# Kernel optimization log

Measured on AMD Instinct MI355X. Metric: run time of the kernel, lower is better.

The kernel has to match this reference:

```python
import jax, jax.numpy as jnp
import numpy as np

N, E = 50000, 800000
IN, HID, HEADS, OUT = 128, 32, 8, 40
D1 = HID * HEADS  # 256


def setup_inputs() -> dict:
    key = jax.random.key(0)
    ks = jax.random.split(key, 24)

    def w(k, fin, fout):
        return (jax.random.normal(k, (fin, fout), jnp.float32) / np.sqrt(fin)).astype(jnp.float32)

    def b(k, fout):
        return (jax.random.normal(k, (fout,), jnp.float32) * 0.02).astype(jnp.float32)

    inp = {
        "x": jax.random.normal(ks[0], (N, IN), jnp.float32),
        "edge_index": jax.random.randint(ks[1], (2, E), 0, N, dtype=jnp.int64),
        # layer 1: TransformerConv(IN -> HID, heads=HEADS, concat=True, beta=True)
        "q1w": w(ks[2], IN, D1), "q1b": b(ks[3], D1),
        "k1w": w(ks[4], IN, D1), "k1b": b(ks[5], D1),
        "v1w": w(ks[6], IN, D1), "v1b": b(ks[7], D1),
        "s1w": w(ks[8], IN, D1), "s1b": b(ks[9], D1),
        "b1w": w(ks[10], 3 * D1, 1),
        # layer 2: TransformerConv(D1 -> OUT, heads=1, concat=False, beta=True)
        "q2w": w(ks[11], D1, OUT), "q2b": b(ks[12], OUT),
        "k2w": w(ks[13], D1, OUT), "k2b": b(ks[14], OUT),
        "v2w": w(ks[15], D1, OUT), "v2b": b(ks[16], OUT),
        "s2w": w(ks[17], D1, OUT), "s2b": b(ks[18], OUT),
        "b2w": w(ks[19], 3 * OUT, 1),
    }
    return inp


def _tconv(x, src, dst, qw, qb, kw, kb, vw, vb, sw, sb, bw, heads, ch, concat):
    """PyG TransformerConv (no edge_attr, root_weight=True, beta=True), eval mode."""
    n = x.shape[0]
    q = (x @ qw + qb).reshape(n, heads, ch)
    k = (x @ kw + kb).reshape(n, heads, ch)
    v = (x @ vw + vb).reshape(n, heads, ch)
    # per-edge attention logits: message flows src(j) -> dst(i)
    alpha = jnp.einsum("ehc,ehc->eh", q[dst], k[src]) / np.sqrt(ch)  # [E,H]
    # segment softmax over incoming edges of each dst node
    amax = jax.ops.segment_max(alpha, dst, num_segments=n)  # [N,H]
    a = jnp.exp(alpha - amax[dst])
    asum = jax.ops.segment_sum(a, dst, num_segments=n)  # [N,H]
    attn = a / asum[dst]  # [E,H]
    # scatter-aggregate weighted values
    out = jax.ops.segment_sum(v[src] * attn[:, :, None], dst, num_segments=n)  # [N,H,C]
    out = out.reshape(n, heads * ch) if concat else out.mean(axis=1)
    skip = x @ sw + sb
    beta = jax.nn.sigmoid(jnp.concatenate([out, skip, out - skip], axis=-1) @ bw)  # [N,1]
    return beta * skip + (1.0 - beta) * out


def reference(x, edge_index, q1w, q1b, k1w, k1b, v1w, v1b, s1w, s1b, b1w,
              q2w, q2b, k2w, k2b, v2w, v2b, s2w, s2b, b2w):
    src, dst = edge_index[0], edge_index[1]
    h = jax.nn.elu(_tconv(x, src, dst, q1w, q1b, k1w, k1b, v1w, v1b, s1w, s1b, b1w, HEADS, HID, True))
    return _tconv(h, src, dst, q2w, q2b, k2w, k2b, v2w, v2b, s2w, s2b, b2w, 1, OUT, False)
```

## Files before the change

kernel.cpp:

```cpp
#include <hip/hip_runtime.h>
#include <cstdint>
#include <cstddef>

#define N_NODES 50000
#define N_EDGES 800000
#define IN_F    128
#define HID     32
#define HEADS   8
#define OUT_F   40
#define D1      256
#define W1COLS  1024
#define W2COLS  160
#define CAP     64

#define GFILL_B   3125
#define G1_BX     391
#define G1_BY     8
#define G1_GEMM_B (G1_BX * G1_BY)
#define G1_TOTAL  (GFILL_B + G1_GEMM_B)

typedef unsigned short ushortT;
typedef unsigned char  ucharT;
typedef unsigned long long ullT;
typedef unsigned short ushortx8 __attribute__((ext_vector_type(8)));
typedef __bf16 bf16x8 __attribute__((ext_vector_type(8)));
typedef float floatx4 __attribute__((ext_vector_type(4)));
typedef float floatx2 __attribute__((ext_vector_type(2)));

__device__ inline ushortT f2bf(float f) {
    union { float f; unsigned int u; } c; c.f = f;
    unsigned int r = c.u + 0x7FFFu + ((c.u >> 16) & 1u);
    return (ushortT)(r >> 16);
}
__device__ inline float bf2f(ushortT h) {
    union { unsigned int u; float f; } c; c.u = ((unsigned int)h) << 16; return c.f;
}

__device__ inline void g2lds16(const void* gptr, void* lptr) {
    __builtin_amdgcn_global_load_lds(
        (const __attribute__((address_space(1))) unsigned int*)gptr,
        (__attribute__((address_space(3))) unsigned int*)lptr,
        16, 0, 0);
}

#define PREP_CONV_B  6250
#define PREP_W1_B    512
#define PREP_W2_B    160
#define PREP_TOTAL_B (PREP_CONV_B + PREP_W1_B + PREP_W2_B)

__global__ __launch_bounds__(256) void k_prep(
        const float* __restrict__ x, ushortT* __restrict__ xb,
        const float* __restrict__ q1w, const float* __restrict__ k1w,
        const float* __restrict__ v1w, const float* __restrict__ s1w,
        const float* __restrict__ q1b, const float* __restrict__ k1b,
        const float* __restrict__ v1b, const float* __restrict__ s1b,
        ushortT* __restrict__ W1T, float* __restrict__ b1c,
        const float* __restrict__ q2w, const float* __restrict__ k2w,
        const float* __restrict__ v2w, const float* __restrict__ s2w,
        const float* __restrict__ q2b, const float* __restrict__ k2b,
        const float* __restrict__ v2b, const float* __restrict__ s2b,
        ushortT* __restrict__ W2T, float* __restrict__ b2c) {
    int b = blockIdx.x;
    int tid = threadIdx.x;
    if (b < PREP_CONV_B) {
        int i = b * 256 + tid;
        float4 v = reinterpret_cast<const float4*>(x)[i];
        ushort4 o;
        o.x = f2bf(v.x); o.y = f2bf(v.y); o.z = f2bf(v.z); o.w = f2bf(v.w);
        reinterpret_cast<ushort4*>(xb)[i] = o;
    } else if (b < PREP_CONV_B + PREP_W1_B) {
        int t = (b - PREP_CONV_B) * 256 + tid;
        int c = t / IN_F, k = t % IN_F;
        int sel = c >> 8, cc = c & 255;
        const float* w = sel == 0 ? q1w : sel == 1 ? k1w : sel == 2 ? v1w : s1w;
        W1T[(size_t)c * IN_F + k] = f2bf(w[(size_t)k * D1 + cc]);
        if (k == 0) {
            const float* bb = sel == 0 ? q1b : sel == 1 ? k1b : sel == 2 ? v1b : s1b;
            b1c[c] = bb[cc];
        }
    } else {
        int t = (b - PREP_CONV_B - PREP_W1_B) * 256 + tid;
        int c = t / D1, k = t % D1;
        int sel = c / OUT_F, cc = c % OUT_F;
        const float* w = sel == 0 ? q2w : sel == 1 ? k2w : sel == 2 ? v2w : s2w;
        W2T[(size_t)c * D1 + k] = f2bf(w[(size_t)k * OUT_F + cc]);
        if (k == 0) {
            const float* bb = sel == 0 ? q2b : sel == 1 ? k2b : sel == 2 ? v2b : s2b;
            b2c[c] = bb[cc];
        }
    }
}

template<int MODE>
__global__ __launch_bounds__(256) void gemm_mfma_pack(
        const ushortT* __restrict__ A, const ushortT* __restrict__ BT,
        const float* __restrict__ bias, float* __restrict__ QSf,
        ushortT* __restrict__ QSh, ucharT* __restrict__ KV8,
        ushortT* __restrict__ K2V2,
        const int* __restrict__ ei, int* __restrict__ cursor, int* __restrict__ col,
        int M, int K, int Nn) {
    constexpr int TM = 128, TN = 128, TK = 32;
    __shared__ float smemf[4 * 1088];
    ushortT* As = reinterpret_cast<ushortT*>(smemf);
    ushortT* Bs = As + TM * TK;
    int bx2, by2;
    if (MODE == 1) {
        int t = blockIdx.x;
        int idx;
        bool isFill;
        if (t < 2 * GFILL_B) { isFill = !(t & 1); idx = t >> 1; }
        else                 { isFill = false;    idx = t - GFILL_B; }
        if (isFill) {
            int e = idx * 256 + threadIdx.x;
            if (e < N_EDGES) {
                int dd = ei[N_EDGES + e];
                int p = atomicAdd(&cursor[dd], 1);
                col[dd * CAP + p] = ei[e];
            }
            return;
        }
        bx2 = idx / G1_BY;
        by2 = idx % G1_BY;
    } else {
        bx2 = blockIdx.x;
        by2 = blockIdx.y;
    }
    int tid = threadIdx.x;
    int lane = tid & 63, wave = tid >> 6;
    int bm = bx2 * TM, bn = by2 * TN;
    int wm = (wave & 1) * 64, wn = (wave >> 1) * 64;
    int mrow = lane & 15, g = lane >> 4;
    int wbase = tid & ~63;
    int rsA0 = min(bm + (tid >> 2), M - 1);
    int rsA1 = min(bm + ((256 + tid) >> 2), M - 1);
    int rsB0 = min(bn + (tid >> 2), Nn - 1);
    int rsB1 = min(bn + ((256 + tid) >> 2), Nn - 1);
    int cs = (tid & 3) * 8;
    floatx4 acc[4][4] = {};

    for (int k0 = 0; k0 < K; k0 += TK) {
        g2lds16(A + (size_t)rsA0 * K + k0 + cs, (char*)As + (size_t)wbase * 16);
        g2lds16(A + (size_t)rsA1 * K + k0 + cs, (char*)As + (size_t)(256 + wbase) * 16);
        g2lds16(BT + (size_t)rsB0 * K + k0 + cs, (char*)Bs + (size_t)wbase * 16);
        g2lds16(BT + (size_t)rsB1 * K + k0 + cs, (char*)Bs + (size_t)(256 + wbase) * 16);
        __syncthreads();
        {
            bf16x8 a[4], b[4];
#pragma unroll
            for (int i = 0; i < 4; ++i)
                a[i] = *reinterpret_cast<const bf16x8*>(As + (wm + i * 16 + mrow) * TK + g * 8);
#pragma unroll
            for (int j = 0; j < 4; ++j)
                b[j] = *reinterpret_cast<const bf16x8*>(Bs + (wn + j * 16 + mrow) * TK + g * 8);
#pragma unroll
            for (int i = 0; i < 4; ++i)
#pragma unroll
                for (int j = 0; j < 4; ++j)
                    acc[i][j] = __builtin_amdgcn_mfma_f32_16x16x32_bf16(a[i], b[j], acc[i][j], 0, 0, 0);
        }
        __syncthreads();
    }

    if (MODE == 1) {
        float* lds = smemf + wave * 1088;
        int sec = by2 >> 1;
        int ccbase = (by2 & 1) * 128 + wn;
        int cb4 = (lane & 15) * 4;
        int rlo = lane >> 4;
        float4 bv = *reinterpret_cast<const float4*>(bias + by2 * 128 + wn + cb4);
#pragma unroll
        for (int i = 0; i < 4; ++i) {
#pragma unroll
            for (int j = 0; j < 4; ++j)
#pragma unroll
                for (int r = 0; r < 4; ++r)
                    lds[(g * 4 + r) * 68 + j * 16 + mrow] = acc[i][j][r];
#pragma unroll
            for (int it = 0; it < 4; ++it) {
                int row = it * 4 + rlo;
                int gm = bm + wm + i * 16 + row;
                if (gm >= M) continue;
                float4 v = *reinterpret_cast<float4*>(lds + row * 68 + cb4);
                v.x += bv.x; v.y += bv.y; v.z += bv.z; v.w += bv.w;
                int cc = ccbase + cb4;
                if (sec == 0 || sec == 3) {
                    ushort4 h;
                    h.x = f2bf(v.x); h.y = f2bf(v.y); h.z = f2bf(v.z); h.w = f2bf(v.w);
                    ushortT* dst = QSh + (size_t)gm * 512 + (sec == 3 ? 256 : 0) + cc;
                    *reinterpret_cast<ushort4*>(dst) = h;
                } else {
                    unsigned int pk = 0;
                    pk = __builtin_amdgcn_cvt_pk_fp8_f32(v.x, v.y, pk, false);
                    pk = __builtin_amdgcn_cvt_pk_fp8_f32(v.z, v.w, pk, true);
                    ucharT* dst = KV8 + (size_t)gm * 512 + (sec == 2 ? 256 : 0) + cc;
                    *reinterpret_cast<unsigned int*>(dst) = pk;
                }
            }
        }
    } else {
#pragma unroll
        for (int i = 0; i < 4; ++i) {
#pragma unroll
            for (int j = 0; j < 4; ++j) {
                int gn = bn + wn + j * 16 + mrow;
                if (gn >= Nn) continue;
                float bvs = bias[gn];
#pragma unroll
                for (int r = 0; r < 4; ++r) {
                    int gm = bm + wm + i * 16 + g * 4 + r;
                    if (gm >= M) continue;
                    float val = acc[i][j][r] + bvs;
                    int sec = gn / OUT_F, cc = gn % OUT_F;
                    if (sec == 0)      QSf[(size_t)gm * 80 + cc] = val;
                    else if (sec == 1) K2V2[(size_t)gm * 80 + cc] = f2bf(val);
                    else if (sec == 2) K2V2[(size_t)gm * 80 + 40 + cc] = f2bf(val);
                    else               QSf[(size_t)gm * 80 + 40 + cc] = val;
                }
            }
        }
    }
}

__global__ __launch_bounds__(256) void k_edge1(
        const ushortT* __restrict__ QSh, const ucharT* __restrict__ KV8,
        const float* __restrict__ bw,
        const int* __restrict__ degc, const int* __restrict__ col,
        ushortT* __restrict__ H1b) {
    int gid  = blockIdx.x * blockDim.x + threadIdx.x;
    int lane = threadIdx.x & 63;
    int node = __builtin_amdgcn_readfirstlane(gid >> 6);
    if (node >= N_NODES) return;
    const float scale = 0.17677669529663687f;
    bool isV = lane >= 32;
    ushortx8 qs8 = *reinterpret_cast<const ushortx8*>(QSh + (size_t)node * 512 + lane * 8);
    float qsc = isV ? 1.0f : scale;
    floatx2 q01, q23, q45, q67;
    q01[0] = bf2f(qs8[0]) * qsc; q01[1] = bf2f(qs8[1]) * qsc;
    q23[0] = bf2f(qs8[2]) * qsc; q23[1] = bf2f(qs8[3]) * qsc;
    q45[0] = bf2f(qs8[4]) * qsc; q45[1] = bf2f(qs8[5]) * qsc;
    q67[0] = bf2f(qs8[6]) * qsc; q67[1] = bf2f(qs8[7]) * qsc;

    float l = 0.f;
    floatx2 acc0 = {0.f, 0.f}, acc1 = {0.f, 0.f}, acc2 = {0.f, 0.f}, acc3 = {0.f, 0.f};
    const int* colp = col + node * CAP;
    int d = degc[node];
    int voff = lane * 8;

#define EDGE_BODY(kv) do {                                                              \
    floatx2 a0 = __builtin_amdgcn_cvt_pk_f32_fp8((unsigned)(kv), false);                \
    floatx2 a1 = __builtin_amdgcn_cvt_pk_f32_fp8((unsigned)(kv), true);                 \
    floatx2 a2 = __builtin_amdgcn_cvt_pk_f32_fp8((unsigned)((kv) >> 32), false);        \
    floatx2 a3 = __builtin_amdgcn_cvt_pk_f32_fp8((unsigned)((kv) >> 32), true);         \
    floatx2 pd = q01 * a0 + q23 * a1 + q45 * a2 + q67 * a3;                             \
    float p = pd[0] + pd[1];                                                            \
    p += __int_as_float(__builtin_amdgcn_update_dpp(                                    \
             0, __float_as_int(p), 0xB1, 0xF, 0xF, false));    \
    p += __int_as_float(__builtin_amdgcn_update_dpp(                                    \
             0, __float_as_int(p), 0x4E, 0xF, 0xF, false));    \
    float e = __expf(p);                                                                \
    float eb = __shfl(e, lane & 31);             \
    l += eb;                                                                            \
    floatx2 ev = {eb, eb};                                                              \
    acc0 += ev * a0; acc1 += ev * a1; acc2 += ev * a2; acc3 += ev * a3;                 \
} while (0)

    int t = 0;
    for (; t + 4 <= d; t += 4) {
        int4 js = *reinterpret_cast<const int4*>(colp + t);
        ullT kv0 = *reinterpret_cast<const ullT*>(KV8 + ((size_t)js.x << 9) + voff);
        ullT kv1 = *reinterpret_cast<const ullT*>(KV8 + ((size_t)js.y << 9) + voff);
        ullT kv2 = *reinterpret_cast<const ullT*>(KV8 + ((size_t)js.z << 9) + voff);
        ullT kv3 = *reinterpret_cast<const ullT*>(KV8 + ((size_t)js.w << 9) + voff);
        EDGE_BODY(kv0);
        EDGE_BODY(kv1);
        EDGE_BODY(kv2);
        EDGE_BODY(kv3);
    }
    for (; t < d; ++t) {
        int j = colp[t];
        ullT kv = *reinterpret_cast<const ullT*>(KV8 + ((size_t)j << 9) + voff);
        EDGE_BODY(kv);
    }
#undef EDGE_BODY

    float inv = (l > 0.f) ? 1.f / l : 0.f;
    floatx2 iv = {inv, inv};
    floatx2 o0 = acc0 * iv, o1 = acc1 * iv, o2 = acc2 * iv, o3 = acc3 * iv;
    int cb = isV ? (lane - 32) * 8 : 0;
    float4 wa0 = *reinterpret_cast<const float4*>(bw + cb);
    float4 wa1 = *reinterpret_cast<const float4*>(bw + cb + 4);
    float4 wb0 = *reinterpret_cast<const float4*>(bw + D1 + cb);
    float4 wb1 = *reinterpret_cast<const float4*>(bw + D1 + cb + 4);
    float4 wc0 = *reinterpret_cast<const float4*>(bw + 2 * D1 + cb);
    float4 wc1 = *reinterpret_cast<const float4*>(bw + 2 * D1 + cb + 4);
    float part = 0.f;
    if (isV) {
        part = o0[0] * wa0.x + o0[1] * wa0.y + o1[0] * wa0.z + o1[1] * wa0.w
             + o2[0] * wa1.x + o2[1] * wa1.y + o3[0] * wa1.z + o3[1] * wa1.w
             + q01[0] * wb0.x + q01[1] * wb0.y + q23[0] * wb0.z + q23[1] * wb0.w
             + q45[0] * wb1.x + q45[1] * wb1.y + q67[0] * wb1.z + q67[1] * wb1.w
             + (o0[0] - q01[0]) * wc0.x + (o0[1] - q01[1]) * wc0.y
             + (o1[0] - q23[0]) * wc0.z + (o1[1] - q23[1]) * wc0.w
             + (o2[0] - q45[0]) * wc1.x + (o2[1] - q45[1]) * wc1.y
             + (o3[0] - q67[0]) * wc1.z + (o3[1] - q67[1]) * wc1.w;
    }
#pragma unroll
    for (int s = 1; s < 32; s <<= 1) part += __shfl_xor(part, s);
    float beta = 1.f / (1.f + __expf(-part));
    if (isV) {
        float h[8];
        h[0] = beta * q01[0] + (1.f - beta) * o0[0];
        h[1] = beta * q01[1] + (1.f - beta) * o0[1];
        h[2] = beta * q23[0] + (1.f - beta) * o1[0];
        h[3] = beta * q23[1] + (1.f - beta) * o1[1];
        h[4] = beta * q45[0] + (1.f - beta) * o2[0];
        h[5] = beta * q45[1] + (1.f - beta) * o2[1];
        h[6] = beta * q67[0] + (1.f - beta) * o3[0];
        h[7] = beta * q67[1] + (1.f - beta) * o3[1];
        ushortx8 hb;
#pragma unroll
        for (int c = 0; c < 8; ++c) {
            float hv = h[c] > 0.f ? h[c] : __expf(h[c]) - 1.f;
            hb[c] = f2bf(hv);
        }
        *reinterpret_cast<ushortx8*>(H1b + (size_t)node * D1 + (lane - 32) * 8) = hb;
    }
}

__global__ __launch_bounds__(256) void k_edge2(
        const float* __restrict__ QS, const ushortT* __restrict__ K2V2,
        const float* __restrict__ bw,
        const int* __restrict__ degc, const int* __restrict__ col,
        float* __restrict__ out) {
    __shared__ float        qbuf[4][40];
    __shared__ float        attn[4][64];
    __shared__ int          jb[4][64];
    __shared__ unsigned int ksm[4][64 * 21];
    int gid  = blockIdx.x * blockDim.x + threadIdx.x;
    int node = gid >> 6;
    int wave = threadIdx.x >> 6;
    int lane = threadIdx.x & 63;
    if (node >= N_NODES) return;
    const float scale = 0.15811388300841897f;
    bool act = lane < OUT_F;
    if (act) qbuf[wave][lane] = QS[(size_t)node * 80 + lane] * scale;

    int d = degc[node];
    if (lane < d) jb[wave][lane] = col[node * CAP + lane];

    const unsigned int* Kdw = reinterpret_cast<const unsigned int*>(K2V2);
    int sr = lane / 20;
    int sc = lane - sr * 20;
    for (int r0 = 0; r0 < d; r0 += 3) {
        int rr = r0 + sr;
        if (lane < 60 && rr < d)
            ksm[wave][rr * 21 + sc] = Kdw[(size_t)jb[wave][rr] * 40 + sc];
    }

    float p = 0.f;
    if (lane < d) {
        float s = 0.f;
#pragma unroll
        for (int c = 0; c < 20; ++c) {
            unsigned int kk = ksm[wave][lane * 21 + c];
            s += qbuf[wave][2 * c]     * bf2f((ushortT)(kk & 0xFFFFu))
               + qbuf[wave][2 * c + 1] * bf2f((ushortT)(kk >> 16));
        }
        p = __expf(s);
    }
    attn[wave][lane] = p;
    float l = p;
#pragma unroll
    for (int s = 1; s < 64; s <<= 1) l += __shfl_xor(l, s);

    float acc = 0.f;
    int ln = act ? lane : 0;
    int e = 0;
    for (; e + 4 <= d; e += 4) {
        int je0 = jb[wave][e],     je1 = jb[wave][e + 1];
        int je2 = jb[wave][e + 2], je3 = jb[wave][e + 3];
        float v0 = bf2f(K2V2[(size_t)je0 * 80 + 40 + ln]);
        float v1 = bf2f(K2V2[(size_t)je1 * 80 + 40 + ln]);
        float v2 = bf2f(K2V2[(size_t)je2 * 80 + 40 + ln]);
        float v3 = bf2f(K2V2[(size_t)je3 * 80 + 40 + ln]);
        acc += (attn[wave][e] * v0 + attn[wave][e + 1] * v1)
             + (attn[wave][e + 2] * v2 + attn[wave][e + 3] * v3);
    }
    for (; e < d; ++e)
        acc += attn[wave][e] * bf2f(K2V2[(size_t)jb[wave][e] * 80 + 40 + ln]);

    float inv = (l > 0.f) ? 1.f / l : 0.f;
    float o  = acc * inv;
    float sk = act ? QS[(size_t)node * 80 + 40 + lane] : 0.f;
    float part = act ? (o * bw[lane] + sk * bw[OUT_F + lane] + (o - sk) * bw[2 * OUT_F + lane]) : 0.f;
#pragma unroll
    for (int s = 1; s < 64; s <<= 1) part += __shfl_xor(part, s);
    float beta = 1.f / (1.f + __expf(-part));
    if (act) out[(size_t)node * OUT_F + lane] = beta * sk + (1.f - beta) * o;
}

extern "C" void kernel_launch(void* const* d_in, const int* in_sizes, int n_in,
                              void* d_out, int out_size, void* d_ws, size_t ws_size,
                              hipStream_t stream) {
    const float* x   = (const float*)d_in[0];
    const int*   ei  = (const int*)d_in[1];
    const float* q1w = (const float*)d_in[2];
    const float* q1b = (const float*)d_in[3];
    const float* k1w = (const float*)d_in[4];
    const float* k1b = (const float*)d_in[5];
    const float* v1w = (const float*)d_in[6];
    const float* v1b = (const float*)d_in[7];
    const float* s1w = (const float*)d_in[8];
    const float* s1b = (const float*)d_in[9];
    const float* b1w = (const float*)d_in[10];
    const float* q2w = (const float*)d_in[11];
    const float* q2b = (const float*)d_in[12];
    const float* k2w = (const float*)d_in[13];
    const float* k2b = (const float*)d_in[14];
    const float* v2w = (const float*)d_in[15];
    const float* v2b = (const float*)d_in[16];
    const float* s2w = (const float*)d_in[17];
    const float* s2b = (const float*)d_in[18];
    const float* b2w = (const float*)d_in[19];
    float* out = (float*)d_out;

    char* w = (char*)d_ws;
    ushortT* QSh = (ushortT*)w;
    ucharT*  KV8 = (ucharT*)(w + 51200000);
    ushortT* H1b = (ushortT*)(w + 102400000);
    ushortT* xb  = (ushortT*)(w + 128000000);
    ushortT* W1T = (ushortT*)(w + 140800000);
    ushortT* W2T = (ushortT*)(w + 141062144);
    float*   b1c = (float*)(w + 141144064);
    float*   b2c = (float*)(w + 141148160);
    int* cursor  = (int*)(w + 141149184);
    int* col     = cursor + N_NODES;
    float*   QS2  = (float*)w;
    ushortT* K2V2 = (ushortT*)(w + 51200000);

    hipMemsetAsync(cursor, 0, N_NODES * sizeof(int), stream);

    k_prep<<<PREP_TOTAL_B, 256, 0, stream>>>(
        x, xb,
        q1w, k1w, v1w, s1w, q1b, k1b, v1b, s1b, W1T, b1c,
        q2w, k2w, v2w, s2w, q2b, k2b, v2b, s2b, W2T, b2c);

    gemm_mfma_pack<1><<<G1_TOTAL, 256, 0, stream>>>(
        xb, W1T, b1c, nullptr, QSh, KV8, nullptr,
        ei, cursor, col, N_NODES, IN_F, W1COLS);

    k_edge1<<<(N_NODES * 64) / 256, 256, 0, stream>>>(QSh, KV8, b1w, cursor, col, H1b);

    dim3 g2((N_NODES + 127) / 128, (W2COLS + 127) / 128);
    gemm_mfma_pack<2><<<g2, 256, 0, stream>>>(H1b, W2T, b2c, QS2, nullptr, nullptr,
                                              K2V2, nullptr, nullptr, nullptr,
                                              N_NODES, D1, W2COLS);

    k_edge2<<<(N_NODES * 64) / 256, 256, 0, stream>>>(QS2, K2V2, b2w, cursor, col, out);
}
```

Before: 344.3 us.

## Double-buffer LDS tiles in MFMA GEMM to overlap global loads with compute

The GEMM main loop now uses two LDS buffers. It issues the next K-tile's global-to-LDS loads before computing on the current tile, using explicit vmcnt waits and raw s_barrier calls in place of __syncthreads. It also hoists the bias load ahead of the loop and precomputes the row base pointers. This is meant to hide global memory latency behind MFMA work, at the cost of twice the LDS per block, which may lower occupancy, and of fragile manual waitcnt ordering.

```diff
diff --git a/kernel.cpp b/kernel.cpp
--- a/kernel.cpp
+++ b/kernel.cpp
@@ -100,9 +100,7 @@
         const int* __restrict__ ei, int* __restrict__ cursor, int* __restrict__ col,
         int M, int K, int Nn) {
     constexpr int TM = 128, TN = 128, TK = 32;
-    __shared__ float smemf[4 * 1088];
-    ushortT* As = reinterpret_cast<ushortT*>(smemf);
-    ushortT* Bs = As + TM * TK;
+    __shared__ float smemf[8192];
     int bx2, by2;
     if (MODE == 1) {
         int t = blockIdx.x;
@@ -136,15 +134,40 @@
     int rsB0 = min(bn + (tid >> 2), Nn - 1);
     int rsB1 = min(bn + ((256 + tid) >> 2), Nn - 1);
     int cs = (tid & 3) * 8;
+    const ushortT* pA0 = A + (size_t)rsA0 * K + cs;
+    const ushortT* pA1 = A + (size_t)rsA1 * K + cs;
+    const ushortT* pB0 = BT + (size_t)rsB0 * K + cs;
+    const ushortT* pB1 = BT + (size_t)rsB1 * K + cs;
+
+    int cb4 = (lane & 15) * 4;
+    float4 bv = make_float4(0.f, 0.f, 0.f, 0.f);
+    if (MODE == 1) bv = *reinterpret_cast<const float4*>(bias + by2 * 128 + wn + cb4);
+
+    auto stage = [&](int sel, int k0) {
+        char* base = (char*)smemf + sel * 16384;
+        g2lds16(pA0 + k0, base + (size_t)wbase * 16);
+        g2lds16(pA1 + k0, base + (size_t)(256 + wbase) * 16);
+        g2lds16(pB0 + k0, base + 8192 + (size_t)wbase * 16);
+        g2lds16(pB1 + k0, base + 8192 + (size_t)(256 + wbase) * 16);
+    };
+
+    int nt = K / TK;
     floatx4 acc[4][4] = {};
-
-    for (int k0 = 0; k0 < K; k0 += TK) {
-        g2lds16(A + (size_t)rsA0 * K + k0 + cs, (char*)As + (size_t)wbase * 16);
-        g2lds16(A + (size_t)rsA1 * K + k0 + cs, (char*)As + (size_t)(256 + wbase) * 16);
-        g2lds16(BT + (size_t)rsB0 * K + k0 + cs, (char*)Bs + (size_t)wbase * 16);
-        g2lds16(BT + (size_t)rsB1 * K + k0 + cs, (char*)Bs + (size_t)(256 + wbase) * 16);
-        __syncthreads();
+    stage(0, 0);
+    for (int t = 0; t < nt; ++t) {
+        if (t + 1 < nt) {
+            stage((t + 1) & 1, (t + 1) * TK);
+            __builtin_amdgcn_sched_barrier(0);
+            asm volatile("s_waitcnt vmcnt(4)" ::: "memory");
+        } else {
+            __builtin_amdgcn_sched_barrier(0);
+            asm volatile("s_waitcnt vmcnt(0)" ::: "memory");
+        }
+        __builtin_amdgcn_s_barrier();
+        __builtin_amdgcn_sched_barrier(0);
         {
+            const ushortT* As = (const ushortT*)((char*)smemf + (t & 1) * 16384);
+            const ushortT* Bs = As + TM * TK;
             bf16x8 a[4], b[4];
 #pragma unroll
             for (int i = 0; i < 4; ++i)
@@ -158,16 +181,15 @@
                 for (int j = 0; j < 4; ++j)
                     acc[i][j] = __builtin_amdgcn_mfma_f32_16x16x32_bf16(a[i], b[j], acc[i][j], 0, 0, 0);
         }
-        __syncthreads();
+        __builtin_amdgcn_sched_barrier(0);
+        __builtin_amdgcn_s_barrier();
     }
 
     if (MODE == 1) {
         float* lds = smemf + wave * 1088;
         int sec = by2 >> 1;
         int ccbase = (by2 & 1) * 128 + wn;
-        int cb4 = (lane & 15) * 4;
         int rlo = lane >> 4;
-        float4 bv = *reinterpret_cast<const float4*>(bias + by2 * 128 + wn + cb4);
 #pragma unroll
         for (int i = 0; i < 4; ++i) {
 #pragma unroll
```

After: 324.0 us. 1.06x faster.
